# Optimization experiments

Measured on AMD Instinct MI355X. Metric: run time of the kernel, lower is better.

Reference implementation:

```python
import jax, jax.numpy as jnp
import numpy as np

B, N, F_IN, H = 16, 1024, 64, 256
NEG = -9e15
ALPHA = 0.2  # LeakyReLU slope


def _leaky(x):
    return jnp.where(x >= 0, x, ALPHA * x)


def setup_inputs() -> dict:
    key = jax.random.key(0)
    ks = jax.random.split(key, 12)
    s = lambda k, shape, fan: jax.random.normal(k, shape, jnp.float32) / np.sqrt(fan)
    node_features = jax.random.normal(ks[0], (B, N, F_IN), jnp.float32)
    adj_matrix = jax.random.randint(ks[1], (B, N, N), 0, 2).astype(jnp.float32)
    return {
        "node_features": node_features,
        "adj_matrix": adj_matrix,
        "emb_W": s(ks[2], (F_IN, H), F_IN),
        "emb_b": jnp.zeros((H,), jnp.float32),
        "W0": s(ks[3], (H, H), H),
        "a1_0": s(ks[4], (H,), H),
        "a2_0": s(ks[5], (H,), H),
        "W1": s(ks[6], (H, H), H),
        "a1_1": s(ks[7], (H,), H),
        "a2_1": s(ks[8], (H,), H),
        "gp_W1": s(ks[9], (H, H), H),
        "gp_b1": jnp.zeros((H,), jnp.float32),
        "gp_W2": s(ks[10], (H, H), H),
        "gp_b2": jnp.zeros((H,), jnp.float32),
    }


def _gat_layer(x, mask, W, a1, a2):
    # x: [B,N,H]; mask: [B,N,N] bool. Equivalent to original concat trick:
    # a([h_i || h_j]) = h_i @ a1 + h_j @ a2 with a.weight split in halves.
    h = jnp.einsum('bnf,fo->bno', x, W)              # [B,N,H]
    s1 = jnp.einsum('bnh,h->bn', h, a1)              # [B,N]
    s2 = jnp.einsum('bnh,h->bn', h, a2)              # [B,N]
    e = _leaky(s1[:, :, None] + s2[:, None, :])      # [B,N,N]
    att = jax.nn.softmax(jnp.where(mask, e, NEG), axis=2)
    # dropout p=0.2 is identity in eval mode
    return jnp.einsum('bij,bjh->bih', att, h)        # [B,N,H]


def reference(node_features, adj_matrix, emb_W, emb_b,
              W0, a1_0, a2_0, W1, a1_1, a2_1,
              gp_W1, gp_b1, gp_W2, gp_b2):
    mask = adj_matrix > 0
    x = jnp.einsum('bnf,fh->bnh', node_features, emb_W) + emb_b
    x = jax.nn.relu(_gat_layer(x, mask, W0, a1_0, a2_0))
    x = jax.nn.relu(_gat_layer(x, mask, W1, a1_1, a2_1))
    g = jnp.mean(x, axis=1) + jnp.max(x, axis=1)     # [B,H]
    g = jax.nn.relu(g @ gp_W1 + gp_b1) @ gp_W2 + gp_b2
    return x, g
```

## Files before the change

kernel.cpp:

```cpp
#include <hip/hip_runtime.h>
#include <hip/hip_bf16.h>

#define B 16
#define N 1024
#define F_IN 64
#define H 256
#define ALPHA 0.2f
#define LOG2E 1.44269504f

typedef __attribute__((ext_vector_type(8))) _Float16 half8;
typedef __attribute__((ext_vector_type(4))) _Float16 half4;
typedef __attribute__((ext_vector_type(4))) float floatx4;
typedef __attribute__((ext_vector_type(16))) float floatx16;

#if __has_builtin(__builtin_amdgcn_exp2f)
#define EXP2F(x) __builtin_amdgcn_exp2f(x)
#else
#define EXP2F(x) exp2f(x)
#endif

__device__ __forceinline__ floatx4 mfma_f16(half8 a, half8 b, floatx4 c) {
    return __builtin_amdgcn_mfma_f32_16x16x32_f16(a, b, c, 0, 0, 0);
}
__device__ __forceinline__ floatx16 mfma32_f16(half8 a, half8 b, floatx16 c) {
    return __builtin_amdgcn_mfma_f32_32x32x16_f16(a, b, c, 0, 0, 0);
}

__global__ __launch_bounds__(256) void k_front(const float* __restrict__ adj,
                                               const float* __restrict__ nf,
                                               const float* __restrict__ embW,
                                               const float* __restrict__ embB,
                                               const float* __restrict__ W0, const float* __restrict__ W1,
                                               const float* __restrict__ a10, const float* __restrict__ a20,
                                               const float* __restrict__ a11, const float* __restrict__ a21,
                                               unsigned* __restrict__ mask32,
                                               _Float16* __restrict__ xf,
                                               _Float16* __restrict__ wBf,
                                               float* __restrict__ wa1, float* __restrict__ wa2) {
    __shared__ float lds[256 * 17];
    const int blk = blockIdx.x;
    const int t = threadIdx.x;
    const int lane = t & 63;

    if (blk < 1024) {
        const int wv = blk * 4 + (t >> 6);
#pragma unroll 2
        for (int task = wv; task < B * N * 4; task += 4096) {
            const float4 v = *(const float4*)(adj + (size_t)task * 256 + lane * 4);
            unsigned long long b0 = __ballot(v.x > 0.f);
            unsigned long long b1 = __ballot(v.y > 0.f);
            unsigned long long b2 = __ballot(v.z > 0.f);
            unsigned long long b3 = __ballot(v.w > 0.f);
            if (lane < 8) {
                unsigned w0 = (unsigned)((b0 >> (8 * lane)) & 0xff)
                            | ((unsigned)((b1 >> (8 * lane)) & 0xff) << 8)
                            | ((unsigned)((b2 >> (8 * lane)) & 0xff) << 16)
                            | ((unsigned)((b3 >> (8 * lane)) & 0xff) << 24);
                const int jg = task & 3, row = task >> 2;
                mask32[(size_t)row * 32 + jg * 8 + lane] = w0;
            }
        }
        return;
    }
    if (blk < 1536) {
        const int row0 = (blk - 1024) * 32;
        float* nfs = lds;
        for (int idx = t; idx < 32 * F_IN; idx += 256) {
            int r = idx >> 6, f = idx & 63;
            nfs[f * 32 + r] = nf[(size_t)(row0 + r) * F_IN + f];
        }
        __syncthreads();
        const int c = t;
        float acc[32];
        const float bv = embB[c];
#pragma unroll
        for (int r = 0; r < 32; r++) acc[r] = bv;
#pragma unroll 8
        for (int f = 0; f < F_IN; f++) {
            const float w = embW[f * H + c];
            const float* nrow = nfs + f * 32;
#pragma unroll
            for (int q = 0; q < 8; q++) {
                float4 n4 = *(const float4*)(nrow + q * 4);
                acc[q * 4 + 0] += n4.x * w;
                acc[q * 4 + 1] += n4.y * w;
                acc[q * 4 + 2] += n4.z * w;
                acc[q * 4 + 3] += n4.w * w;
            }
        }
#pragma unroll
        for (int r = 0; r < 32; r++)
            xf[(size_t)(row0 + r) * H + c] = (_Float16)acc[r];
        return;
    }
    const int pb = blk - 1536;
    if (pb >= 32) {
        const int l = pb - 32;
        const float* W = l ? W1 : W0;
        const float* a1 = l ? a11 : a10;
        const float* a2 = l ? a21 : a20;
        float* a1s = lds;
        float* a2s = lds + 256;
        a1s[t] = a1[t]; a2s[t] = a2[t];
        __syncthreads();
        float v1 = 0.f, v2 = 0.f;
        for (int c = 0; c < H; c += 4) {
            float4 w = *(const float4*)&W[t * H + c];
            v1 += w.x * a1s[c] + w.y * a1s[c + 1] + w.z * a1s[c + 2] + w.w * a1s[c + 3];
            v2 += w.x * a2s[c] + w.y * a2s[c + 1] + w.z * a2s[c + 2] + w.w * a2s[c + 3];
        }
        wa1[l * H + t] = v1;
        wa2[l * H + t] = v2;
        return;
    }
    const int l = pb >> 4, ct = pb & 15;
    const float* W = l ? W1 : W0;
#pragma unroll
    for (int rep = 0; rep < 16; rep++) {
        int idx = rep * 256 + t;
        int k = idx >> 4, cl = idx & 15;
        lds[k * 17 + cl] = W[k * H + ct * 16 + cl];
    }
    __syncthreads();
    const int w = t >> 6;
    const int l15 = lane & 15, quad = lane >> 4;
#pragma unroll
    for (int e = 0; e < 2; e++) {
        const int ks = w * 2 + e;
        half8 bf;
#pragma unroll
        for (int jj = 0; jj < 8; jj++)
            bf[jj] = (_Float16)lds[(ks * 32 + quad * 8 + jj) * 17 + l15];
        *(half8*)(wBf + (size_t)(((l * 16 + ct) * 8 + ks) * 64 + lane) * 8) = bf;
    }
}

#define XS(it, ks) ((((it) * 8 + (ks))) * 520)
__global__ __launch_bounds__(256, 4) void k_gemm(const _Float16* __restrict__ xf,
                                                 const _Float16* __restrict__ wBf,
                                                 const float* __restrict__ wa1, const float* __restrict__ wa2,
                                                 _Float16* __restrict__ hB,
                                                 float* __restrict__ s1, float* __restrict__ s2) {
    __shared__ __align__(16) _Float16 sm[8320];
    const int lin = blockIdx.x;
    const int rc = lin >> 1, chalf = lin & 1;
    const int row0 = rc * 32;
    const int t = threadIdx.x;
    const int lane = t & 63, w = t >> 6;
    const int l15 = lane & 15, quad = lane >> 4;

#pragma unroll
    for (int pass = 0; pass < 4; pass++) {
        int idx = pass * 256 + t;
        int row_l = idx >> 5, k8 = idx & 31;
        half8 v = *(const half8*)(xf + (size_t)(row0 + row_l) * H + k8 * 8);
        int it = row_l >> 4, lf = row_l & 15, ks = k8 >> 2, qd = k8 & 3;
        *(half8*)(sm + XS(it, ks) + (qd * 16 + lf) * 8) = v;
    }
    __syncthreads();

    const int ct0 = chalf * 8 + 2 * w;
    const _Float16* pB0 = wBf + (size_t)((ct0 * 8) * 64 + lane) * 8;
    const _Float16* pB1 = wBf + (size_t)(((ct0 + 1) * 8) * 64 + lane) * 8;

    floatx4 acc[2][2];
    floatx4 z = {0.f, 0.f, 0.f, 0.f};
    acc[0][0] = z; acc[0][1] = z; acc[1][0] = z; acc[1][1] = z;
    float sp1a = 0.f, sp2a = 0.f, sp1b = 0.f, sp2b = 0.f;

    half8 B0 = *(const half8*)(pB0);
    half8 B1 = *(const half8*)(pB1);

#pragma unroll
    for (int ks = 0; ks < 8; ks++) {
        half8 nB0 = B0, nB1 = B1;
        if (ks < 7) {
            const int o = (ks + 1) * 512;
            nB0 = *(const half8*)(pB0 + o);
            nB1 = *(const half8*)(pB1 + o);
        }
        half8 A0 = *(const half8*)(sm + XS(0, ks) + lane * 8);
        half8 A1 = *(const half8*)(sm + XS(1, ks) + lane * 8);
        acc[0][0] = mfma_f16(A0, B0, acc[0][0]);
        acc[0][1] = mfma_f16(A0, B1, acc[0][1]);
        acc[1][0] = mfma_f16(A1, B0, acc[1][0]);
        acc[1][1] = mfma_f16(A1, B1, acc[1][1]);
        if (chalf == 0 && w == 0) {
            float4 w1a = *(const float4*)(wa1 + ks * 32 + quad * 8);
            float4 w1b = *(const float4*)(wa1 + ks * 32 + quad * 8 + 4);
            float4 w2a = *(const float4*)(wa2 + ks * 32 + quad * 8);
            float4 w2b = *(const float4*)(wa2 + ks * 32 + quad * 8 + 4);
            float wv1[8] = {w1a.x, w1a.y, w1a.z, w1a.w, w1b.x, w1b.y, w1b.z, w1b.w};
            float wv2[8] = {w2a.x, w2a.y, w2a.z, w2a.w, w2b.x, w2b.y, w2b.z, w2b.w};
#pragma unroll
            for (int j = 0; j < 8; j++) {
                float xa = (float)A0[j];
                float xb = (float)A1[j];
                sp1a += xa * wv1[j]; sp2a += xa * wv2[j];
                sp1b += xb * wv1[j]; sp2b += xb * wv2[j];
            }
        }
        B0 = nB0; B1 = nB1;
    }

    __syncthreads();
    _Float16* trc = sm;
#pragma unroll
    for (int rg = 0; rg < 2; rg++) {
#pragma unroll
        for (int n2 = 0; n2 < 2; n2++) {
            const int c_l = (2 * w + n2) * 16 + l15;
            half4 hv;
            hv[0] = (_Float16)acc[rg][n2][0];
            hv[1] = (_Float16)acc[rg][n2][1];
            hv[2] = (_Float16)acc[rg][n2][2];
            hv[3] = (_Float16)acc[rg][n2][3];
            *(half4*)(trc + c_l * 40 + rg * 16 + quad * 4) = hv;
        }
    }
    __syncthreads();
    {
        const int bb = row0 >> 10, jtb = (row0 >> 5) & 31;
#pragma unroll
        for (int rep = 0; rep < 2; rep++) {
            int slot = rep * 256 + t;
            int l = slot & 63, frag = slot >> 6;
            int k4 = frag >> 1, ks = frag & 1;
            int c_l = k4 * 32 + (l & 31);
            int roff = ks * 16 + (l >> 5) * 8;
            half8 hv = *(const half8*)(trc + c_l * 40 + roff);
            _Float16* dst = hB + ((size_t)((bb * 8 + chalf * 4 + k4) * 32 + jtb) * 2 + ks) * 512 + l * 8;
            *(half8*)dst = hv;
        }
    }
    if (chalf == 0 && w == 0) {
        sp1a += __shfl_xor(sp1a, 16); sp1a += __shfl_xor(sp1a, 32);
        sp2a += __shfl_xor(sp2a, 16); sp2a += __shfl_xor(sp2a, 32);
        sp1b += __shfl_xor(sp1b, 16); sp1b += __shfl_xor(sp1b, 32);
        sp2b += __shfl_xor(sp2b, 16); sp2b += __shfl_xor(sp2b, 32);
        if (quad == 0) {
            s1[row0 + l15] = sp1a; s2[row0 + l15] = sp2a;
            s1[row0 + 16 + l15] = sp1b; s2[row0 + 16 + l15] = sp2b;
        }
    }
}

template <int LAST>
__global__ __launch_bounds__(256, 1) void k_gat(const _Float16* __restrict__ hB,
                                                const float* __restrict__ s1g,
                                                const float* __restrict__ s2g,
                                                const unsigned* __restrict__ mask32,
                                                float* __restrict__ outf,
                                                _Float16* __restrict__ oxf,
                                                float* __restrict__ psum, float* __restrict__ pmax) {
    __shared__ float s2s[N];
    __shared__ unsigned msk[128][33];
    __shared__ float wmax[4];
    __shared__ float red1[4][128];
    __shared__ float red2[4][128];
    const int lin = blockIdx.x;
    const int xcd = lin & 7, sl = lin >> 3;
    const int b = xcd * 2 + (sl & 1);
    const int chunk = (sl >> 1) & 7;
    const int chalf = sl >> 4;
    const int i0 = chunk * 128;
    const int t = threadIdx.x;
    const int lane = t & 63, w = t >> 6;
    const int l31 = lane & 31, hi = lane >> 5;
    const int hi2 = hi * 2, hi8 = hi * 8;

    float tm = -INFINITY;
    for (int idx = t; idx < N; idx += 256) {
        float v = s2g[b * N + idx] * LOG2E;
        s2s[idx] = v;
        tm = fmaxf(tm, v);
    }
#pragma unroll
    for (int off = 1; off <= 32; off <<= 1) tm = fmaxf(tm, __shfl_xor(tm, off));
    if (lane == 0) wmax[w] = tm;
#pragma unroll
    for (int pass = 0; pass < 16; pass++) {
        int idx = pass * 256 + t;
        int r = idx >> 5, wd = idx & 31;
        msk[r][wd] = mask32[(size_t)(b * N + i0 + r) * 32 + wd];
    }
    __syncthreads();
    const float s2maxL = fmaxf(fmaxf(wmax[0], wmax[1]), fmaxf(wmax[2], wmax[3]));

    const float s1L = s1g[b * N + i0 + w * 32 + l31] * LOG2E;
    const float tmx = s1L + s2maxL;
    const float mL = fmaxf(tmx, ALPHA * tmx);
    const float a1c = s1L - mL;
    const float a2c = fmaf(ALPHA, s1L, -mL);

    const _Float16* pb[4][2];
#pragma unroll
    for (int k4 = 0; k4 < 4; k4++)
#pragma unroll
        for (int ks = 0; ks < 2; ks++)
            pb[k4][ks] = hB + ((size_t)(b * 8 + chalf * 4 + k4) * 64 + ks) * 512 + lane * 8;

    floatx16 acc[4];
    floatx16 accl;
#pragma unroll
    for (int r = 0; r < 16; r++) accl[r] = 0.f;
#pragma unroll
    for (int k4 = 0; k4 < 4; k4++) acc[k4] = accl;

    half8 ones;
#pragma unroll
    for (int jj = 0; jj < 8; jj++) ones[jj] = (_Float16)1.0f;

    const float* svp = s2s + hi8;
    const unsigned* mr = &msk[w * 32 + l31][0];

    half8 bufA[4][2], bufB[4][2];
#pragma unroll
    for (int k4 = 0; k4 < 4; k4++) {
        bufA[k4][0] = *(const half8*)(pb[k4][0]);
        bufA[k4][1] = *(const half8*)(pb[k4][1]);
    }

#define GAT_STEP(JT, BUF)                                                      \
    do {                                                                       \
        const unsigned m = mr[JT];                                             \
        float4 sa0 = *(const float4*)(svp + (JT) * 32);                        \
        float4 sb0 = *(const float4*)(svp + (JT) * 32 + 4);                    \
        float4 sa1 = *(const float4*)(svp + (JT) * 32 + 16);                   \
        float4 sb1 = *(const float4*)(svp + (JT) * 32 + 20);                   \
        float sv0[8] = {sa0.x, sa0.y, sa0.z, sa0.w, sb0.x, sb0.y, sb0.z, sb0.w};\
        float sv1[8] = {sa1.x, sa1.y, sa1.z, sa1.w, sb1.x, sb1.y, sb1.z, sb1.w};\
        unsigned mq0 = m >> hi2;                                               \
        unsigned mq1 = m >> (4 + hi2);                                         \
        union { _Float16 h[8]; half8 v; } pk0, pk1;                            \
        _Pragma("unroll")                                                      \
        for (int e = 0; e < 8; e++) {                                          \
            const int bp = (e & 3) * 8 + (e >> 2);                             \
            float u0 = a1c + sv0[e];                                           \
            float v0 = fmaf(ALPHA, sv0[e], a2c);                               \
            float w0 = fmaxf(u0, v0);                                          \
            w0 = ((mq0 >> bp) & 1u) ? w0 : -126.f;                             \
            pk0.h[e] = (_Float16)EXP2F(w0);                                    \
            float u1 = a1c + sv1[e];                                           \
            float v1 = fmaf(ALPHA, sv1[e], a2c);                               \
            float w1 = fmaxf(u1, v1);                                          \
            w1 = ((mq1 >> bp) & 1u) ? w1 : -126.f;                             \
            pk1.h[e] = (_Float16)EXP2F(w1);                                    \
        }                                                                      \
        accl = mfma32_f16(pk0.v, ones, accl);                                  \
        _Pragma("unroll")                                                      \
        for (int k4 = 0; k4 < 4; k4++) acc[k4] = mfma32_f16(pk0.v, BUF[k4][0], acc[k4]); \
        accl = mfma32_f16(pk1.v, ones, accl);                                  \
        _Pragma("unroll")                                                      \
        for (int k4 = 0; k4 < 4; k4++) acc[k4] = mfma32_f16(pk1.v, BUF[k4][1], acc[k4]); \
    } while (0)

    for (int jt = 0; jt < 32; jt += 2) {
        {
            const int o = (jt + 1) * 1024;
#pragma unroll
            for (int k4 = 0; k4 < 4; k4++) {
                bufB[k4][0] = *(const half8*)(pb[k4][0] + o);
                bufB[k4][1] = *(const half8*)(pb[k4][1] + o);
            }
        }
        GAT_STEP(jt, bufA);
        if (jt + 2 < 32) {
            const int o = (jt + 2) * 1024;
#pragma unroll
            for (int k4 = 0; k4 < 4; k4++) {
                bufA[k4][0] = *(const half8*)(pb[k4][0] + o);
                bufA[k4][1] = *(const half8*)(pb[k4][1] + o);
            }
        }
        GAT_STEP(jt + 1, bufB);
    }
#undef GAT_STEP

    float invv[16];
#pragma unroll
    for (int r = 0; r < 16; r++) invv[r] = 1.f / accl[r];

    const size_t rowb = (size_t)b * N + i0 + w * 32 + 4 * hi;
    const int colbase = chalf * 128;
#pragma unroll
    for (int k4 = 0; k4 < 4; k4++) {
        const int c = colbase + k4 * 32 + l31;
        float cs = 0.f, cm = -INFINITY;
#pragma unroll
        for (int reg = 0; reg < 16; reg++) {
            const int roff = (reg & 3) + 8 * (reg >> 2);
            float v = fmaxf(acc[k4][reg] * invv[reg], 0.f);
            if (LAST) {
                outf[(rowb + roff) * H + c] = v;
                cs += v; cm = fmaxf(cm, v);
            } else {
                oxf[(rowb + roff) * H + c] = (_Float16)v;
            }
        }
        if (LAST) {
            cs += __shfl_xor(cs, 32);
            cm = fmaxf(cm, __shfl_xor(cm, 32));
            if (hi == 0) { red1[w][k4 * 32 + l31] = cs; red2[w][k4 * 32 + l31] = cm; }
        }
    }
    if (LAST) {
        __syncthreads();
        if (t < 128) {
            float s = red1[0][t] + red1[1][t] + red1[2][t] + red1[3][t];
            float m = fmaxf(fmaxf(red2[0][t], red2[1][t]), fmaxf(red2[2][t], red2[3][t]));
            psum[(b * 8 + chunk) * H + chalf * 128 + t] = s;
            pmax[(b * 8 + chunk) * H + chalf * 128 + t] = m;
        }
    }
}

__global__ __launch_bounds__(256) void k_pool2(const float* __restrict__ psum,
                                               const float* __restrict__ pmax,
                                               const float* __restrict__ W1, const float* __restrict__ b1,
                                               const float* __restrict__ W2, const float* __restrict__ b2,
                                               float* __restrict__ gout) {
    __shared__ float g_s[H];
    __shared__ float t_s[H];
    const int b = blockIdx.x;
    const int c = threadIdx.x;
    float s = 0.f, m = -INFINITY;
#pragma unroll
    for (int ch = 0; ch < 8; ch++) {
        s += psum[(b * 8 + ch) * H + c];
        m = fmaxf(m, pmax[(b * 8 + ch) * H + c]);
    }
    g_s[c] = s * (1.f / N) + m;
    __syncthreads();
    float a = b1[c];
#pragma unroll 16
    for (int k = 0; k < H; k++) a += g_s[k] * W1[k * H + c];
    t_s[c] = fmaxf(a, 0.f);
    __syncthreads();
    float o = b2[c];
#pragma unroll 16
    for (int k = 0; k < H; k++) o += t_s[k] * W2[k * H + c];
    gout[b * H + c] = o;
}

extern "C" void kernel_launch(void* const* d_in, const int* in_sizes, int n_in,
                              void* d_out, int out_size, void* d_ws, size_t ws_size,
                              hipStream_t stream) {
    const float* nf    = (const float*)d_in[0];
    const float* adj   = (const float*)d_in[1];
    const float* emb_W = (const float*)d_in[2];
    const float* emb_b = (const float*)d_in[3];
    const float* W0    = (const float*)d_in[4];
    const float* a1_0  = (const float*)d_in[5];
    const float* a2_0  = (const float*)d_in[6];
    const float* W1    = (const float*)d_in[7];
    const float* a1_1  = (const float*)d_in[8];
    const float* a2_1  = (const float*)d_in[9];
    const float* gpW1  = (const float*)d_in[10];
    const float* gpb1  = (const float*)d_in[11];
    const float* gpW2  = (const float*)d_in[12];
    const float* gpb2  = (const float*)d_in[13];

    float* xout = (float*)d_out;
    float* gout = xout + B * N * H;

    char* w = (char*)d_ws;
    _Float16* xf     = (_Float16*)(w);
    _Float16* hB     = (_Float16*)(w + 8388608);
    unsigned* mask32 = (unsigned*)(w + 16777216);
    float* s1        = (float*)(w + 18874368);
    float* s2        = (float*)(w + 18939904);
    _Float16* wBf    = (_Float16*)(w + 19005440);
    float* wa1       = (float*)(w + 19267584);
    float* wa2       = (float*)(w + 19269632);
    float* psum      = (float*)(w + 19271680);
    float* pmax      = (float*)(w + 19533824);

    k_front<<<1570, 256, 0, stream>>>(adj, nf, emb_W, emb_b, W0, W1,
                                      a1_0, a2_0, a1_1, a2_1,
                                      mask32, xf, wBf, wa1, wa2);

    k_gemm<<<1024, 256, 0, stream>>>(xf, wBf, wa1, wa2, hB, s1, s2);
    k_gat<0><<<256, 256, 0, stream>>>(hB, s1, s2, mask32, nullptr, xf,
                                      nullptr, nullptr);

    k_gemm<<<1024, 256, 0, stream>>>(xf, wBf + 65536, wa1 + H, wa2 + H, hB, s1, s2);
    k_gat<1><<<256, 256, 0, stream>>>(hB, s1, s2, mask32, xout, nullptr,
                                      psum, pmax);

    k_pool2<<<B, 256, 0, stream>>>(psum, pmax, gpW1, gpb1, gpW2, gpb2, gout);
}
```

Before: 221.3 us.

## Fuse embedding projection into first GEMM using MFMA instead of front kernel

Moves the node-feature embedding (nf @ emb_W + b) out of the front kernel and into the first k_gemm. Each GEMM block now recomputes its 32-row slice of embeddings in LDS with f16 MFMA, using emb_W prepacked into fragments by one front block. This removes the fp32 scalar embedding blocks and the global write and read of the intermediate xf for layer 0. Each of the two column-half blocks per row chunk redoes the embedding, and nf is rounded to f16 before the multiply.

```diff
diff --git a/kernel.cpp b/kernel.cpp
--- a/kernel.cpp
+++ b/kernel.cpp
@@ -27,15 +27,13 @@
 }
 
 __global__ __launch_bounds__(256) void k_front(const float* __restrict__ adj,
-                                               const float* __restrict__ nf,
                                                const float* __restrict__ embW,
-                                               const float* __restrict__ embB,
                                                const float* __restrict__ W0, const float* __restrict__ W1,
                                                const float* __restrict__ a10, const float* __restrict__ a20,
                                                const float* __restrict__ a11, const float* __restrict__ a21,
                                                unsigned* __restrict__ mask32,
-                                               _Float16* __restrict__ xf,
                                                _Float16* __restrict__ wBf,
+                                               _Float16* __restrict__ embf,
                                                float* __restrict__ wa1, float* __restrict__ wa2) {
     __shared__ float lds[256 * 17];
     const int blk = blockIdx.x;
@@ -62,38 +60,20 @@
         }
         return;
     }
-    if (blk < 1536) {
-        const int row0 = (blk - 1024) * 32;
-        float* nfs = lds;
-        for (int idx = t; idx < 32 * F_IN; idx += 256) {
-            int r = idx >> 6, f = idx & 63;
-            nfs[f * 32 + r] = nf[(size_t)(row0 + r) * F_IN + f];
-        }
-        __syncthreads();
-        const int c = t;
-        float acc[32];
-        const float bv = embB[c];
-#pragma unroll
-        for (int r = 0; r < 32; r++) acc[r] = bv;
-#pragma unroll 8
-        for (int f = 0; f < F_IN; f++) {
-            const float w = embW[f * H + c];
-            const float* nrow = nfs + f * 32;
-#pragma unroll
-            for (int q = 0; q < 8; q++) {
-                float4 n4 = *(const float4*)(nrow + q * 4);
-                acc[q * 4 + 0] += n4.x * w;
-                acc[q * 4 + 1] += n4.y * w;
-                acc[q * 4 + 2] += n4.z * w;
-                acc[q * 4 + 3] += n4.w * w;
-            }
-        }
-#pragma unroll
-        for (int r = 0; r < 32; r++)
-            xf[(size_t)(row0 + r) * H + c] = (_Float16)acc[r];
+    const int pb = blk - 1024;
+    if (pb == 34) {
+        for (int s = t; s < 2048; s += 256) {
+            const int ln = s & 63, ct2 = s >> 6;
+            const int ct = ct2 >> 1, ks2 = ct2 & 1;
+            const int q = ln >> 4, lw = ln & 15;
+            half8 bf;
+#pragma unroll
+            for (int e = 0; e < 8; e++)
+                bf[e] = (_Float16)embW[(ks2 * 32 + q * 8 + e) * H + ct * 16 + lw];
+            *(half8*)(embf + (size_t)s * 8) = bf;
+        }
         return;
     }
-    const int pb = blk - 1536;
     if (pb >= 32) {
         const int l = pb - 32;
         const float* W = l ? W1 : W0;
@@ -136,7 +116,11 @@
 }
 
 #define XS(it, ks) ((((it) * 8 + (ks))) * 520)
+template <int EMB>
 __global__ __launch_bounds__(256, 4) void k_gemm(const _Float16* __restrict__ xf,
+                                                 const float* __restrict__ nf,
+                                                 const _Float16* __restrict__ embf,
+                                                 const float* __restrict__ embB,
                                                  const _Float16* __restrict__ wBf,
                                                  const float* __restrict__ wa1, const float* __restrict__ wa2,
                                                  _Float16* __restrict__ hB,
@@ -149,13 +133,49 @@
     const int lane = t & 63, w = t >> 6;
     const int l15 = lane & 15, quad = lane >> 4;
 
-#pragma unroll
-    for (int pass = 0; pass < 4; pass++) {
-        int idx = pass * 256 + t;
-        int row_l = idx >> 5, k8 = idx & 31;
-        half8 v = *(const half8*)(xf + (size_t)(row0 + row_l) * H + k8 * 8);
-        int it = row_l >> 4, lf = row_l & 15, ks = k8 >> 2, qd = k8 & 3;
-        *(half8*)(sm + XS(it, ks) + (qd * 16 + lf) * 8) = v;
+    if (EMB) {
+        half8 anf[2][2];
+#pragma unroll
+        for (int it = 0; it < 2; it++)
+#pragma unroll
+            for (int ks2 = 0; ks2 < 2; ks2++) {
+                const float* src = nf + (size_t)(row0 + it * 16 + l15) * F_IN + ks2 * 32 + quad * 8;
+                float4 f0 = *(const float4*)(src);
+                float4 f1 = *(const float4*)(src + 4);
+                half8 a;
+                a[0] = (_Float16)f0.x; a[1] = (_Float16)f0.y;
+                a[2] = (_Float16)f0.z; a[3] = (_Float16)f0.w;
+                a[4] = (_Float16)f1.x; a[5] = (_Float16)f1.y;
+                a[6] = (_Float16)f1.z; a[7] = (_Float16)f1.w;
+                anf[it][ks2] = a;
+            }
+#pragma unroll
+        for (int ctl = 0; ctl < 4; ctl++) {
+            const int ct = w * 4 + ctl;
+            half8 be0 = *(const half8*)(embf + (size_t)((ct * 2 + 0) * 64 + lane) * 8);
+            half8 be1 = *(const half8*)(embf + (size_t)((ct * 2 + 1) * 64 + lane) * 8);
+            const int col = ct * 16 + l15;
+            const float bias = embB[col];
+            const int ks = col >> 5, qd = (col >> 3) & 3, e = col & 7;
+#pragma unroll
+            for (int it = 0; it < 2; it++) {
+                floatx4 xa = {0.f, 0.f, 0.f, 0.f};
+                xa = mfma_f16(anf[it][0], be0, xa);
+                xa = mfma_f16(anf[it][1], be1, xa);
+#pragma unroll
+                for (int r = 0; r < 4; r++)
+                    sm[XS(it, ks) + (qd * 16 + quad * 4 + r) * 8 + e] = (_Float16)(xa[r] + bias);
+            }
+        }
+    } else {
+#pragma unroll
+        for (int pass = 0; pass < 4; pass++) {
+            int idx = pass * 256 + t;
+            int row_l = idx >> 5, k8 = idx & 31;
+            half8 v = *(const half8*)(xf + (size_t)(row0 + row_l) * H + k8 * 8);
+            int it = row_l >> 4, lf = row_l & 15, ks = k8 >> 2, qd = k8 & 3;
+            *(half8*)(sm + XS(it, ks) + (qd * 16 + lf) * 8) = v;
+        }
     }
     __syncthreads();
 
@@ -475,16 +495,19 @@
     float* wa2       = (float*)(w + 19269632);
     float* psum      = (float*)(w + 19271680);
     float* pmax      = (float*)(w + 19533824);
-
-    k_front<<<1570, 256, 0, stream>>>(adj, nf, emb_W, emb_b, W0, W1,
+    _Float16* embf   = (_Float16*)(w + 19795968);
+
+    k_front<<<1059, 256, 0, stream>>>(adj, emb_W, W0, W1,
                                       a1_0, a2_0, a1_1, a2_1,
-                                      mask32, xf, wBf, wa1, wa2);
-
-    k_gemm<<<1024, 256, 0, stream>>>(xf, wBf, wa1, wa2, hB, s1, s2);
+                                      mask32, wBf, embf, wa1, wa2);
+
+    k_gemm<1><<<1024, 256, 0, stream>>>(nullptr, nf, embf, emb_b,
+                                        wBf, wa1, wa2, hB, s1, s2);
     k_gat<0><<<256, 256, 0, stream>>>(hB, s1, s2, mask32, nullptr, xf,
                                       nullptr, nullptr);
 
-    k_gemm<<<1024, 256, 0, stream>>>(xf, wBf + 65536, wa1 + H, wa2 + H, hB, s1, s2);
+    k_gemm<0><<<1024, 256, 0, stream>>>(xf, nullptr, nullptr, nullptr,
+                                        wBf + 65536, wa1 + H, wa2 + H, hB, s1, s2);
     k_gat<1><<<256, 256, 0, stream>>>(hB, s1, s2, mask32, xout, nullptr,
                                       psum, pmax);
 
```

Result: no change. 219.0 us (median of 2 runs) (-1.0%).
